# Performance work log

Hardware: AMD Instinct MI355X
Metric: run time of the kernel (lower is better)

## Reference

```python
import jax, jax.numpy as jnp
import numpy as np

B, S, E = 4, 2048, 512
Q, FFN = 8, 2048


def setup_inputs() -> dict:
    key = jax.random.key(0)
    k_x, k_th, k_w1, k_w2 = jax.random.split(key, 4)
    x = jax.random.normal(k_x, (B, S, E), dtype=jnp.float32)
    # trainable RY angles, one per wire
    theta = jax.random.normal(k_th, (Q,), dtype=jnp.float32)
    W1 = jax.random.normal(k_w1, (Q, FFN), dtype=jnp.float32) / np.sqrt(Q)
    b1 = jnp.zeros((FFN,), dtype=jnp.float32)
    W2 = jax.random.normal(k_w2, (FFN, E), dtype=jnp.float32) / np.sqrt(FFN)
    b2 = jnp.zeros((E,), dtype=jnp.float32)
    return {"x": x, "theta": theta, "W1": W1, "b1": b1, "W2": W2, "b2": b2}


def reference(x, theta, W1, b1, W2, b2):
    # Quantum circuit: |0> -> RX(x_i) -> RY(theta_i) -> <Z> per wire.
    # No entangling gates, so the 8-qubit state factorizes; simulate each
    # qubit's 2 complex amplitudes, batched over all tokens & wires at once.
    n_wires = theta.shape[0]
    xq = x[..., :n_wires]                     # encoder uses input_idx 0..7: [B,S,Q]
    # RX(x)|0> = cos(x/2)|0> - i sin(x/2)|1>
    a = jnp.cos(xq * 0.5).astype(jnp.complex64)
    b = (-1j) * jnp.sin(xq * 0.5).astype(jnp.complex64)
    # RY(theta) = [[c,-s],[s,c]], c=cos(theta/2), s=sin(theta/2)
    c = jnp.cos(theta * 0.5).astype(jnp.complex64)
    s = jnp.sin(theta * 0.5).astype(jnp.complex64)
    a2 = c * a - s * b
    b2_ = s * a + c * b
    # <Z> = |amp0|^2 - |amp1|^2  -> [B,S,Q]
    z = (jnp.abs(a2) ** 2 - jnp.abs(b2_) ** 2).astype(x.dtype)
    # dropout is identity at inference
    h = jax.nn.relu(jnp.einsum('bsq,qf->bsf', z, W1) + b1)
    return jnp.einsum('bsf,fe->bse', h, W2) + b2
```

## Files before the change

### kernel.cpp

```cpp
#include <hip/hip_runtime.h>
#include <hip/hip_bf16.h>

typedef __bf16 bf16_t;
typedef __bf16 bf16x4 __attribute__((ext_vector_type(4)));
typedef __bf16 bf16x8 __attribute__((ext_vector_type(8)));
typedef float f32x4 __attribute__((ext_vector_type(4)));

#define M_TOT 8192
#define N_TOT 512
#define K_TOT 2048
#define E_TOT 512
#define NSEG  16

__device__ __forceinline__ bf16x8 zero8() {
    bf16x8 v;
#pragma unroll
    for (int i = 0; i < 8; ++i) v[i] = (bf16_t)0.0f;
    return v;
}

__global__ __launch_bounds__(256)
void prep4_kernel(const float* __restrict__ x,
                  const float* __restrict__ theta,
                  const float* __restrict__ W1,
                  const float* __restrict__ b1,
                  const float* __restrict__ W2,
                  bf16_t* __restrict__ W2t,
                  bf16_t* __restrict__ zb,
                  bf16_t* __restrict__ W1p)
{
    const int b = blockIdx.x;
    if (b < 256) {
        __shared__ bf16_t T[64][66];
        const int k0 = (b >> 3) * 64;
        const int n0 = (b & 7) * 64;
        const int kl = threadIdx.x >> 4;
        const int n4 = threadIdx.x & 15;
#pragma unroll
        for (int i = 0; i < 4; ++i) {
            int k = kl + i * 16;
            float4 v = *(const float4*)(W2 + (size_t)(k0 + k) * N_TOT + n0 + n4 * 4);
            T[n4 * 4 + 0][k] = (bf16_t)v.x;
            T[n4 * 4 + 1][k] = (bf16_t)v.y;
            T[n4 * 4 + 2][k] = (bf16_t)v.z;
            T[n4 * 4 + 3][k] = (bf16_t)v.w;
        }
        __syncthreads();
        const int nl = threadIdx.x >> 4;
        const int k4 = threadIdx.x & 15;
#pragma unroll
        for (int i = 0; i < 4; ++i) {
            int n = nl + i * 16;
            bf16x4 v;
            v[0] = T[n][k4 * 4 + 0];
            v[1] = T[n][k4 * 4 + 1];
            v[2] = T[n][k4 * 4 + 2];
            v[3] = T[n][k4 * 4 + 3];
            *(bf16x4*)(W2t + (size_t)(n0 + n) * K_TOT + k0 + k4 * 4) = v;
        }
    } else if (b < 288) {
        const int m = (b - 256) * 256 + threadIdx.x;
        float4 x0 = *(const float4*)(x + (size_t)m * E_TOT);
        float4 x1 = *(const float4*)(x + (size_t)m * E_TOT + 4);
        float xs[8] = {x0.x, x0.y, x0.z, x0.w, x1.x, x1.y, x1.z, x1.w};
        bf16x8 lo;
#pragma unroll
        for (int q = 0; q < 8; ++q)
            lo[q] = (bf16_t)(__builtin_cosf(theta[q]) * __builtin_cosf(xs[q]));
        bf16x8 hi = zero8();
        hi[0] = (bf16_t)1.0f;
        *(bf16x8*)(zb + (size_t)m * 16)     = lo;
        *(bf16x8*)(zb + (size_t)m * 16 + 8) = hi;
    } else {
        const int d  = (b - 288) * 256 + threadIdx.x;
        const int c  = d >> 5;
        const int dd = d & 31;
        const int p  = dd >> 4;
        const int rr = dd & 15;
        const int f  = c * 32 + ((rr >> 2) << 3) + (p << 2) + (rr & 3);
        bf16x8 lo;
#pragma unroll
        for (int q = 0; q < 8; ++q)
            lo[q] = (bf16_t)W1[(size_t)q * K_TOT + f];
        bf16x8 hi = zero8();
        hi[0] = (bf16_t)b1[f];
        *(bf16x8*)(W1p + (size_t)d * 16)     = lo;
        *(bf16x8*)(W1p + (size_t)d * 16 + 8) = hi;
    }
}

__device__ __forceinline__ void load_B(const bf16_t* __restrict__ W2t, int n_base,
                                       int k0, int t, uint4 gv[4]) {
#pragma unroll
    for (int j = 0; j < 4; ++j) {
        int s    = t + j * 256;
        int tile = s >> 9;
        int n    = (s >> 3) & 63;
        int g    = (s & 7) ^ (n & 7);
        gv[j] = *(const uint4*)(W2t + (size_t)(n_base + n) * K_TOT
                                + k0 + tile * 64 + g * 8);
    }
}
__device__ __forceinline__ void write_B(bf16_t* Bb, int t, const uint4 gv[4]) {
#pragma unroll
    for (int j = 0; j < 4; ++j) {
        int s    = t + j * 256;
        int tile = s >> 9;
        int n    = (s >> 3) & 63;
        int seg  = s & 7;
        *(uint4*)(Bb + tile * 4096 + n * 64 + seg * 8) = gv[j];
    }
}

__device__ __forceinline__ void load_wf(const bf16_t* __restrict__ W1p, int k0,
                                        int l15, int lq, bf16x8 wf[4]) {
#pragma unroll
    for (int i = 0; i < 4; ++i) wf[i] = zero8();
    if (lq < 2) {
        const int base = (k0 >> 5) * 2;
#pragma unroll
        for (int i = 0; i < 4; ++i)
            wf[i] = *(const bf16x8*)(W1p + (size_t)((base + i) * 16 + l15) * 16 + lq * 8);
    }
}

__device__ __forceinline__ void compute_tile(const bf16_t* Bb, const bf16x8 wf[4],
                                             const bf16x8 zfrag[2],
                                             int l15, int lq,
                                             f32x4 acc[2][4]) {
    bf16x8 bfr[2][4];
#pragma unroll
    for (int c = 0; c < 2; ++c)
#pragma unroll
        for (int nt = 0; nt < 4; ++nt) {
            int r = nt * 16 + l15;
            int s = (c * 4 + lq) ^ (r & 7);
            bfr[c][nt] = *(const bf16x8*)(Bb + r * 64 + s * 8);
        }

    bf16x8 af[2][2];
#pragma unroll
    for (int mt = 0; mt < 2; ++mt)
#pragma unroll
        for (int c = 0; c < 2; ++c) {
            f32x4 h0 = (f32x4){0.f, 0.f, 0.f, 0.f};
            f32x4 h1 = (f32x4){0.f, 0.f, 0.f, 0.f};
            h0 = __builtin_amdgcn_mfma_f32_16x16x32_bf16(wf[c * 2 + 0], zfrag[mt], h0, 0, 0, 0);
            h1 = __builtin_amdgcn_mfma_f32_16x16x32_bf16(wf[c * 2 + 1], zfrag[mt], h1, 0, 0, 0);
            bf16x8 a;
#pragma unroll
            for (int r = 0; r < 4; ++r) {
                a[r]     = (bf16_t)fmaxf(h0[r], 0.f);
                a[r + 4] = (bf16_t)fmaxf(h1[r], 0.f);
            }
            af[mt][c] = a;
        }

#pragma unroll
    for (int c = 0; c < 2; ++c)
#pragma unroll
        for (int mt = 0; mt < 2; ++mt)
#pragma unroll
            for (int nt = 0; nt < 4; ++nt)
                acc[mt][nt] = __builtin_amdgcn_mfma_f32_16x16x32_bf16(
                    af[mt][c], bfr[c][nt], acc[mt][nt], 0, 0, 0);
}

__global__ __launch_bounds__(256, 2)
void ffq_gemm_kernel(const bf16_t* __restrict__ zb,
                     const bf16_t* __restrict__ W1p,
                     const bf16_t* __restrict__ W2t,
                     const float* __restrict__ b2,
                     float* __restrict__ out)
{
    __shared__ bf16_t Blds[2][2 * 64 * 64];

    const int t = threadIdx.x;
    const int w = t >> 6, l = t & 63;
    const int m_base = blockIdx.y * 128;
    const int n_base = blockIdx.x * 64;
    const int wm = w;
    const int l15 = l & 15, lq = l >> 4;

    bf16x8 zfrag[2];
#pragma unroll
    for (int mt = 0; mt < 2; ++mt) {
        zfrag[mt] = zero8();
        if (lq < 2)
            zfrag[mt] = *(const bf16x8*)(zb + (size_t)(m_base + wm * 32 + mt * 16 + l15) * 16 + lq * 8);
    }

    f32x4 acc[2][4];
#pragma unroll
    for (int mt = 0; mt < 2; ++mt)
#pragma unroll
        for (int nt = 0; nt < 4; ++nt)
            acc[mt][nt] = (f32x4){0.f, 0.f, 0.f, 0.f};

    uint4 gv[4];

    load_B(W2t, n_base, 0, t, gv);
    write_B(Blds[0], t, gv);

    for (int s = 0; s < NSEG; ++s) {
        const int cur = s & 1;
        __syncthreads();
        if (s + 1 < NSEG) load_B(W2t, n_base, (s + 1) * 128, t, gv);

#pragma unroll
        for (int tt = 0; tt < 2; ++tt) {
            bf16x8 wf[4];
            load_wf(W1p, s * 128 + tt * 64, l15, lq, wf);
            compute_tile(Blds[cur] + tt * 4096, wf, zfrag, l15, lq, acc);
        }

        if (s + 1 < NSEG) write_B(Blds[1 - cur], t, gv);
    }

#pragma unroll
    for (int nt = 0; nt < 4; ++nt) {
        int col = n_base + nt * 16 + l15;
        float bias = b2[col];
#pragma unroll
        for (int mt = 0; mt < 2; ++mt) {
#pragma unroll
            for (int r = 0; r < 4; ++r) {
                int row = m_base + wm * 32 + mt * 16 + lq * 4 + r;
                out[(size_t)row * N_TOT + col] = acc[mt][nt][r] + bias;
            }
        }
    }
}

extern "C" void kernel_launch(void* const* d_in, const int* in_sizes, int n_in,
                              void* d_out, int out_size, void* d_ws, size_t ws_size,
                              hipStream_t stream) {
    const float* x     = (const float*)d_in[0];
    const float* theta = (const float*)d_in[1];
    const float* W1    = (const float*)d_in[2];
    const float* b1    = (const float*)d_in[3];
    const float* W2    = (const float*)d_in[4];
    const float* b2    = (const float*)d_in[5];
    float* out = (float*)d_out;

    const size_t W2T_BYTES = (size_t)N_TOT * K_TOT * sizeof(bf16_t);
    const size_t ZB_BYTES  = (size_t)M_TOT * 16 * sizeof(bf16_t);

    bf16_t* W2t = (bf16_t*)d_ws;
    bf16_t* zb  = (bf16_t*)((char*)d_ws + W2T_BYTES);
    bf16_t* W1p = (bf16_t*)((char*)d_ws + W2T_BYTES + ZB_BYTES);

    prep4_kernel<<<296, 256, 0, stream>>>(x, theta, W1, b1, W2, W2t, zb, W1p);

    dim3 grid(N_TOT / 64, M_TOT / 128);
    ffq_gemm_kernel<<<grid, 256, 0, stream>>>(zb, W1p, W2t, b2, out);
}
```

Baseline: 108.5 us.

## Software-pipeline first-GEMM activations one segment ahead with priority boost

Restructures the main loop so the small first-layer MFMA (W1·z + relu) for segment s+1 is computed after segment s's main GEMM. Its W1p fragment loads are issued early, alongside the W2 prefetch, and the h activations are held in ping-pong register sets. The aim is to take the dependent W1 load → MFMA → relu chain off the critical path of each segment. s_setprio raises wave priority during the main MFMA block. The extra live register fragments could hurt occupancy under the 2-wave launch bound.

```diff
diff --git a/kernel.cpp b/kernel.cpp
--- a/kernel.cpp
+++ b/kernel.cpp
@@ -112,58 +112,91 @@
     }
 }
 
-__device__ __forceinline__ void load_wf(const bf16_t* __restrict__ W1p, int k0,
-                                        int l15, int lq, bf16x8 wf[4]) {
-#pragma unroll
-    for (int i = 0; i < 4; ++i) wf[i] = zero8();
-    if (lq < 2) {
-        const int base = (k0 >> 5) * 2;
-#pragma unroll
-        for (int i = 0; i < 4; ++i)
-            wf[i] = *(const bf16x8*)(W1p + (size_t)((base + i) * 16 + l15) * 16 + lq * 8);
-    }
-}
-
-__device__ __forceinline__ void compute_tile(const bf16_t* Bb, const bf16x8 wf[4],
-                                             const bf16x8 zfrag[2],
-                                             int l15, int lq,
-                                             f32x4 acc[2][4]) {
-    bf16x8 bfr[2][4];
-#pragma unroll
-    for (int c = 0; c < 2; ++c)
-#pragma unroll
-        for (int nt = 0; nt < 4; ++nt) {
-            int r = nt * 16 + l15;
-            int s = (c * 4 + lq) ^ (r & 7);
-            bfr[c][nt] = *(const bf16x8*)(Bb + r * 64 + s * 8);
-        }
-
-    bf16x8 af[2][2];
-#pragma unroll
-    for (int mt = 0; mt < 2; ++mt)
-#pragma unroll
-        for (int c = 0; c < 2; ++c) {
-            f32x4 h0 = (f32x4){0.f, 0.f, 0.f, 0.f};
-            f32x4 h1 = (f32x4){0.f, 0.f, 0.f, 0.f};
-            h0 = __builtin_amdgcn_mfma_f32_16x16x32_bf16(wf[c * 2 + 0], zfrag[mt], h0, 0, 0, 0);
-            h1 = __builtin_amdgcn_mfma_f32_16x16x32_bf16(wf[c * 2 + 1], zfrag[mt], h1, 0, 0, 0);
-            bf16x8 a;
-#pragma unroll
-            for (int r = 0; r < 4; ++r) {
-                a[r]     = (bf16_t)fmaxf(h0[r], 0.f);
-                a[r + 4] = (bf16_t)fmaxf(h1[r], 0.f);
+__device__ __forceinline__ void load_wf_seg(const bf16_t* __restrict__ W1p, int s,
+                                            int l15, int lq, bf16x8 wfs[2][4]) {
+#pragma unroll
+    for (int tt = 0; tt < 2; ++tt) {
+        const int base = s * 8 + tt * 4;
+#pragma unroll
+        for (int i = 0; i < 4; ++i) {
+            wfs[tt][i] = zero8();
+            if (lq < 2)
+                wfs[tt][i] = *(const bf16x8*)(W1p + (size_t)((base + i) * 16 + l15) * 16 + lq * 8);
+        }
+    }
+}
+
+__device__ __forceinline__ void compute_h(const bf16x8 wfs[2][4],
+                                          const bf16x8 zfrag[2],
+                                          bf16x8 af[2][2][2]) {
+#pragma unroll
+    for (int tt = 0; tt < 2; ++tt)
+#pragma unroll
+        for (int mt = 0; mt < 2; ++mt)
+#pragma unroll
+            for (int c = 0; c < 2; ++c) {
+                f32x4 h0 = (f32x4){0.f, 0.f, 0.f, 0.f};
+                f32x4 h1 = (f32x4){0.f, 0.f, 0.f, 0.f};
+                h0 = __builtin_amdgcn_mfma_f32_16x16x32_bf16(wfs[tt][c * 2 + 0], zfrag[mt], h0, 0, 0, 0);
+                h1 = __builtin_amdgcn_mfma_f32_16x16x32_bf16(wfs[tt][c * 2 + 1], zfrag[mt], h1, 0, 0, 0);
+                bf16x8 a;
+#pragma unroll
+                for (int r = 0; r < 4; ++r) {
+                    a[r]     = (bf16_t)fmaxf(h0[r], 0.f);
+                    a[r + 4] = (bf16_t)fmaxf(h1[r], 0.f);
+                }
+                af[tt][mt][c] = a;
             }
-            af[mt][c] = a;
-        }
-
-#pragma unroll
-    for (int c = 0; c < 2; ++c)
-#pragma unroll
-        for (int mt = 0; mt < 2; ++mt)
-#pragma unroll
-            for (int nt = 0; nt < 4; ++nt)
-                acc[mt][nt] = __builtin_amdgcn_mfma_f32_16x16x32_bf16(
-                    af[mt][c], bfr[c][nt], acc[mt][nt], 0, 0, 0);
+}
+
+__device__ __forceinline__ void compute_main(const bf16_t* Bb,
+                                             const bf16x8 af[2][2][2],
+                                             int l15, int lq, f32x4 acc[2][4]) {
+#pragma unroll
+    for (int tt = 0; tt < 2; ++tt) {
+        bf16x8 bfr[2][4];
+#pragma unroll
+        for (int c = 0; c < 2; ++c)
+#pragma unroll
+            for (int nt = 0; nt < 4; ++nt) {
+                int r  = nt * 16 + l15;
+                int sm = (c * 4 + lq) ^ (r & 7);
+                bfr[c][nt] = *(const bf16x8*)(Bb + tt * 4096 + r * 64 + sm * 8);
+            }
+#pragma unroll
+        for (int c = 0; c < 2; ++c)
+#pragma unroll
+            for (int mt = 0; mt < 2; ++mt)
+#pragma unroll
+                for (int nt = 0; nt < 4; ++nt)
+                    acc[mt][nt] = __builtin_amdgcn_mfma_f32_16x16x32_bf16(
+                        af[tt][mt][c], bfr[c][nt], acc[mt][nt], 0, 0, 0);
+    }
+}
+
+__device__ __forceinline__ void seg_step(int s, const bf16_t* Bcur, bf16_t* Bnext,
+                                         const bf16_t* __restrict__ W2t,
+                                         const bf16_t* __restrict__ W1p,
+                                         int n_base, int t, int l15, int lq,
+                                         const bf16x8 zfrag[2],
+                                         const bf16x8 af_cur[2][2][2],
+                                         bf16x8 af_nxt[2][2][2],
+                                         f32x4 acc[2][4]) {
+    __syncthreads();
+    uint4 gv[4];
+    bf16x8 wfs[2][4];
+    const bool pre = (s + 1 < NSEG);
+    if (pre) {
+        load_B(W2t, n_base, (s + 1) * 128, t, gv);
+        load_wf_seg(W1p, s + 1, l15, lq, wfs);
+    }
+    __builtin_amdgcn_s_setprio(1);
+    compute_main(Bcur, af_cur, l15, lq, acc);
+    __builtin_amdgcn_s_setprio(0);
+    if (pre) {
+        compute_h(wfs, zfrag, af_nxt);
+        write_B(Bnext, t, gv);
+    }
 }
 
 __global__ __launch_bounds__(256, 2)
@@ -197,24 +230,23 @@
         for (int nt = 0; nt < 4; ++nt)
             acc[mt][nt] = (f32x4){0.f, 0.f, 0.f, 0.f};
 
-    uint4 gv[4];
-
-    load_B(W2t, n_base, 0, t, gv);
-    write_B(Blds[0], t, gv);
-
-    for (int s = 0; s < NSEG; ++s) {
-        const int cur = s & 1;
-        __syncthreads();
-        if (s + 1 < NSEG) load_B(W2t, n_base, (s + 1) * 128, t, gv);
-
-#pragma unroll
-        for (int tt = 0; tt < 2; ++tt) {
-            bf16x8 wf[4];
-            load_wf(W1p, s * 128 + tt * 64, l15, lq, wf);
-            compute_tile(Blds[cur] + tt * 4096, wf, zfrag, l15, lq, acc);
-        }
-
-        if (s + 1 < NSEG) write_B(Blds[1 - cur], t, gv);
+    {
+        uint4 gv0[4];
+        load_B(W2t, n_base, 0, t, gv0);
+        write_B(Blds[0], t, gv0);
+    }
+    bf16x8 afA[2][2][2], afB[2][2][2];
+    {
+        bf16x8 wfs0[2][4];
+        load_wf_seg(W1p, 0, l15, lq, wfs0);
+        compute_h(wfs0, zfrag, afA);
+    }
+
+    for (int sp = 0; sp < NSEG; sp += 2) {
+        seg_step(sp,     Blds[0], Blds[1], W2t, W1p, n_base, t, l15, lq,
+                 zfrag, afA, afB, acc);
+        seg_step(sp + 1, Blds[1], Blds[0], W2t, W1p, n_base, t, l15, lq,
+                 zfrag, afB, afA, acc);
     }
 
 #pragma unroll
```

After: 118.5 us. 9.2% more time.
